# Kernel optimization log

Hardware: AMD Instinct MI355X
Metric: run time of the kernel (lower is better)

## Reference

```python
import jax, jax.numpy as jnp
import numpy as np

VTH = 0.5      # SNNParameters.vth_init
TAU = 0.25     # SNNParameters.tau_mem
_GAUSS_C = 1.0 / np.sqrt(0.3 * np.pi)  # surrogate-grad scale (unused in fwd)


def _heaviside(v):
    return (v > 0).astype(v.dtype)


def setup_inputs() -> dict:
    key = jax.random.key(0)
    x = jax.random.normal(key, (16, 128, 512, 32), dtype=jnp.float32)
    return {"x": x}


def reference(x):
    # x: [..., T]; LIF recurrence over the last (time) axis.
    xT = jnp.moveaxis(x, -1, 0)  # [T, ...]
    u0 = jnp.zeros(x.shape[:-1], dtype=x.dtype)
    o0 = jnp.zeros(x.shape[:-1], dtype=x.dtype)

    def step(carry, x_t):
        u, o_prev = carry
        u = TAU * u * (1.0 - o_prev) + x_t          # leaky integrate w/ reset
        o = _heaviside(u - VTH)                     # fire
        return (u, o), o

    _, outT = jax.lax.scan(step, (u0, o0), xT)
    return jnp.moveaxis(outT, 0, -1)  # back to [..., T]
```

## Files before the change

### kernel.cpp

```cpp
#include <hip/hip_runtime.h>


constexpr int T = 32;
constexpr float TAU = 0.25f;
constexpr float VTH = 0.5f;
constexpr int QUADS_PER_ROW = T / 4;
constexpr int TILE_F4 = 256 * QUADS_PER_ROW;

__device__ __forceinline__ int swz(int s) { return s ^ ((s >> 3) & 7); }

__global__ __launch_bounds__(256) void LIFSpike_kernel(
    const float* __restrict__ x, float* __restrict__ out) {
    __shared__ float4 tile[TILE_F4];

    const int t = threadIdx.x;
    const size_t base = (size_t)blockIdx.x * TILE_F4;

    const float4* __restrict__ xp = reinterpret_cast<const float4*>(x);
#pragma unroll
    for (int k = 0; k < QUADS_PER_ROW; ++k) {
        int s = k * 256 + t;
        tile[swz(s)] = xp[base + s];
    }
    __syncthreads();

    float u = 0.0f, o = 0.0f;
#pragma unroll
    for (int j = 0; j < QUADS_PER_ROW; ++j) {
        int phys = t * QUADS_PER_ROW + (j ^ (t & 7));
        float4 v = tile[phys];
        float4 r;

        u = TAU * u * (1.0f - o) + v.x;
        o = (u > VTH) ? 1.0f : 0.0f;
        r.x = o;

        u = TAU * u * (1.0f - o) + v.y;
        o = (u > VTH) ? 1.0f : 0.0f;
        r.y = o;

        u = TAU * u * (1.0f - o) + v.z;
        o = (u > VTH) ? 1.0f : 0.0f;
        r.z = o;

        u = TAU * u * (1.0f - o) + v.w;
        o = (u > VTH) ? 1.0f : 0.0f;
        r.w = o;

        tile[phys] = r;
    }
    __syncthreads();

    float4* __restrict__ op = reinterpret_cast<float4*>(out);
#pragma unroll
    for (int k = 0; k < QUADS_PER_ROW; ++k) {
        int s = k * 256 + t;
        op[base + s] = tile[swz(s)];
    }
}

extern "C" void kernel_launch(void* const* d_in, const int* in_sizes, int n_in,
                              void* d_out, int out_size, void* d_ws, size_t ws_size,
                              hipStream_t stream) {
    const float* x = (const float*)d_in[0];
    float* out = (float*)d_out;
    int total_f4 = in_sizes[0] / 4;
    int grid = total_f4 / TILE_F4;
    LIFSpike_kernel<<<grid, 256, 0, stream>>>(x, out);
}
```

Measured before the change: 230.4 us.

## Load input directly into LDS per wave and replace block barriers with waitcnts

Input tiles are now copied straight from global memory into shared memory with the global_load_lds builtin, skipping the round trip through registers. Each wave owns a private slice of the tile, and the swizzle moves to the global source address. That lets the two block-wide __syncthreads be replaced by per-wave s_waitcnt vmcnt/lgkmcnt waits. Correctness now depends on LDS ordering within a wave and on the hardware's direct-to-LDS addressing matching the intended layout.

After: 230.8 us. About the same (+0.2%).

```diff
diff --git a/kernel.cpp b/kernel.cpp
--- a/kernel.cpp
+++ b/kernel.cpp
@@ -4,8 +4,10 @@
 constexpr int T = 32;
 constexpr float TAU = 0.25f;
 constexpr float VTH = 0.5f;
-constexpr int QUADS_PER_ROW = T / 4;
-constexpr int TILE_F4 = 256 * QUADS_PER_ROW;
+constexpr int QPR = T / 4;
+constexpr int WAVE_F4 = 64 * QPR;
+constexpr int BLOCK = 256;
+constexpr int TILE_F4 = (BLOCK / 64) * WAVE_F4;
 
 __device__ __forceinline__ int swz(int s) { return s ^ ((s >> 3) & 7); }
 
@@ -14,20 +16,29 @@
     __shared__ float4 tile[TILE_F4];
 
     const int t = threadIdx.x;
+    const int lane = t & 63;
+    const int wid = t >> 6;
+    const int wbase = wid * WAVE_F4;
     const size_t base = (size_t)blockIdx.x * TILE_F4;
 
     const float4* __restrict__ xp = reinterpret_cast<const float4*>(x);
+    float4* __restrict__ op = reinterpret_cast<float4*>(out);
+
 #pragma unroll
-    for (int k = 0; k < QUADS_PER_ROW; ++k) {
-        int s = k * 256 + t;
-        tile[swz(s)] = xp[base + s];
+    for (int k = 0; k < QPR; ++k) {
+        const int p = wbase + k * 64;
+        const int src = swz(p + lane);
+        __builtin_amdgcn_global_load_lds(
+            (const __attribute__((address_space(1))) void*)(xp + base + src),
+            (__attribute__((address_space(3))) void*)(tile + p),
+            16, 0, 0);
     }
-    __syncthreads();
+    asm volatile("s_waitcnt vmcnt(0)" ::: "memory");
 
     float u = 0.0f, o = 0.0f;
 #pragma unroll
-    for (int j = 0; j < QUADS_PER_ROW; ++j) {
-        int phys = t * QUADS_PER_ROW + (j ^ (t & 7));
+    for (int j = 0; j < QPR; ++j) {
+        const int phys = t * QPR + (j ^ (t & 7));
         float4 v = tile[phys];
         float4 r;
 
@@ -49,13 +60,12 @@
 
         tile[phys] = r;
     }
-    __syncthreads();
+    asm volatile("s_waitcnt lgkmcnt(0)" ::: "memory");
 
-    float4* __restrict__ op = reinterpret_cast<float4*>(out);
 #pragma unroll
-    for (int k = 0; k < QUADS_PER_ROW; ++k) {
-        int s = k * 256 + t;
-        op[base + s] = tile[swz(s)];
+    for (int k = 0; k < QPR; ++k) {
+        const int p = wbase + k * 64 + lane;
+        op[base + p] = tile[swz(p)];
     }
 }
 
@@ -66,5 +76,5 @@
     float* out = (float*)d_out;
     int total_f4 = in_sizes[0] / 4;
     int grid = total_f4 / TILE_F4;
-    LIFSpike_kernel<<<grid, 256, 0, stream>>>(x, out);
+    LIFSpike_kernel<<<grid, BLOCK, 0, stream>>>(x, out);
 }
```

## Replace LDS transpose with quad-cooperative shuffle recurrence and persistent grid

Applied to the files above, without the earlier changes.

Drops the shared-memory staging tile. Each group of 4 lanes now loads a 128-byte row directly with coalesced float4 reads and hands the membrane potential serially between lanes with __shfl. The kernel becomes a grid-stride loop over fixed 2048 blocks, and the output uses nontemporal stores. This removes LDS traffic and barriers, but serializes each step through shuffles and leaves 3 of every 4 lanes idle per step, adding latency per chunk.

Result: no change. 232.6 us (+1.0%).

```diff
diff --git a/kernel.cpp b/kernel.cpp
--- a/kernel.cpp
+++ b/kernel.cpp
@@ -1,61 +1,56 @@
 #include <hip/hip_runtime.h>
 
 
-constexpr int T = 32;
 constexpr float TAU = 0.25f;
 constexpr float VTH = 0.5f;
-constexpr int QUADS_PER_ROW = T / 4;
-constexpr int TILE_F4 = 256 * QUADS_PER_ROW;
+constexpr int BLOCK = 256;
+constexpr int GRID = 2048;
 
-__device__ __forceinline__ int swz(int s) { return s ^ ((s >> 3) & 7); }
+typedef float f32x4 __attribute__((ext_vector_type(4)));
 
-__global__ __launch_bounds__(256) void LIFSpike_kernel(
-    const float* __restrict__ x, float* __restrict__ out) {
-    __shared__ float4 tile[TILE_F4];
 
+__global__ __launch_bounds__(BLOCK) void LIFSpike_kernel(
+    const float* __restrict__ x, float* __restrict__ out, int n_chunks) {
     const int t = threadIdx.x;
-    const size_t base = (size_t)blockIdx.x * TILE_F4;
+    const int lane = t & 63;
+    const int j = lane & 3;
+    const int g = lane >> 2;
+    const int wave = blockIdx.x * (BLOCK / 64) + (t >> 6);
+    const int nwaves = gridDim.x * (BLOCK / 64);
 
-    const float4* __restrict__ xp = reinterpret_cast<const float4*>(x);
+    const f32x4* __restrict__ xp = reinterpret_cast<const f32x4*>(x);
+    f32x4* __restrict__ op = reinterpret_cast<f32x4*>(out);
+
+    for (size_t c = wave; c < (size_t)n_chunks; c += nwaves) {
+        const size_t a0 = c * 128 + (size_t)g * 8 + j;
+        const f32x4 v0 = xp[a0];
+        const f32x4 v1 = xp[a0 + 4];
+        f32x4 r0, r1;
+
+        float u = 0.0f, o = 0.0f;
 #pragma unroll
-    for (int k = 0; k < QUADS_PER_ROW; ++k) {
-        int s = k * 256 + t;
-        tile[swz(s)] = xp[base + s];
-    }
-    __syncthreads();
+        for (int s = 0; s < 8; ++s) {
+            if (j == (s & 3)) {
+                const f32x4 v = (s < 4) ? v0 : v1;
+                float uu = u, oo = o;
+                f32x4 r;
+                uu = TAU * uu * (1.0f - oo) + v.x;
+                oo = (uu > VTH) ? 1.0f : 0.0f;  r.x = oo;
+                uu = TAU * uu * (1.0f - oo) + v.y;
+                oo = (uu > VTH) ? 1.0f : 0.0f;  r.y = oo;
+                uu = TAU * uu * (1.0f - oo) + v.z;
+                oo = (uu > VTH) ? 1.0f : 0.0f;  r.z = oo;
+                uu = TAU * uu * (1.0f - oo) + v.w;
+                oo = (uu > VTH) ? 1.0f : 0.0f;  r.w = oo;
+                u = uu;
+                if (s < 4) r0 = r; else r1 = r;
+            }
+            u = __shfl(u, (lane & ~3) | (s & 3));
+            o = (u > VTH) ? 1.0f : 0.0f;
+        }
 
-    float u = 0.0f, o = 0.0f;
-#pragma unroll
-    for (int j = 0; j < QUADS_PER_ROW; ++j) {
-        int phys = t * QUADS_PER_ROW + (j ^ (t & 7));
-        float4 v = tile[phys];
-        float4 r;
-
-        u = TAU * u * (1.0f - o) + v.x;
-        o = (u > VTH) ? 1.0f : 0.0f;
-        r.x = o;
-
-        u = TAU * u * (1.0f - o) + v.y;
-        o = (u > VTH) ? 1.0f : 0.0f;
-        r.y = o;
-
-        u = TAU * u * (1.0f - o) + v.z;
-        o = (u > VTH) ? 1.0f : 0.0f;
-        r.z = o;
-
-        u = TAU * u * (1.0f - o) + v.w;
-        o = (u > VTH) ? 1.0f : 0.0f;
-        r.w = o;
-
-        tile[phys] = r;
-    }
-    __syncthreads();
-
-    float4* __restrict__ op = reinterpret_cast<float4*>(out);
-#pragma unroll
-    for (int k = 0; k < QUADS_PER_ROW; ++k) {
-        int s = k * 256 + t;
-        op[base + s] = tile[swz(s)];
+        __builtin_nontemporal_store(r0, op + a0);
+        __builtin_nontemporal_store(r1, op + a0 + 4);
     }
 }
 
@@ -64,7 +59,6 @@
                               hipStream_t stream) {
     const float* x = (const float*)d_in[0];
     float* out = (float*)d_out;
-    int total_f4 = in_sizes[0] / 4;
-    int grid = total_f4 / TILE_F4;
-    LIFSpike_kernel<<<grid, 256, 0, stream>>>(x, out);
+    int n_chunks = in_sizes[0] / 512;
+    LIFSpike_kernel<<<GRID, BLOCK, 0, stream>>>(x, out, n_chunks);
 }
```
